# Kernel tuning notes

Measured on AMD Instinct MI355X. Metric: run time of the kernel, lower is better.

## Reference

```python
import jax, jax.numpy as jnp
import numpy as np

# Kernel codes matching style 'L;O2;P2;Y2,1,1;R0.5;W1,1'
KERNEL_CODES = ['L', 'O', 'P', 'Y', 'R', 'W']
SM_TEMP = 1.0


def _norm_sq(q, k):
    # q: [n,l,h,e], k: [n,s,h,e] -> [n,h,l,s]
    q2 = jnp.einsum('nlhe,nlhe->nhl', q, q)[..., None]        # [n,h,l,1]
    k2 = jnp.einsum('nshe,nshe->nhs', k, k)[:, :, None, :]     # [n,h,1,s]
    qk = jnp.einsum('nlhe,nshe->nhls', q, k)
    return q2 + k2 - 2.0 * qk


def _kernel(code, q, k):
    if code == 'L':
        return jnp.einsum('nlhe,nshe->nhls', q, k)
    if code == 'O':  # -log(1 + ns^(p/2)), p=2
        return -jnp.log1p(_norm_sq(q, k))
    if code == 'P':  # -(ns)^(p/2), p=2
        return -_norm_sq(q, k)
    if code == 'Y':  # (alpha*<q,k> + c)^p, p=2, alpha=1, c=1
        d = jnp.einsum('nlhe,nshe->nhls', q, k)
        return (d + 1.0) ** 2
    if code == 'R':  # exp(-gamma*ns), gamma=0.5
        return jnp.exp(-0.5 * _norm_sq(q, k))
    if code == 'W':  # cos(ns/a)*exp(-ns/b), a=b=1
        ns = _norm_sq(q, k)
        return jnp.cos(ns) * jnp.exp(-ns)
    raise ValueError(code)


def setup_inputs() -> dict:
    key = jax.random.key(0)
    k1, k2, k3, k4 = jax.random.split(key, 4)
    N, L, S, H, E, K = 2, 1024, 1024, 8, 64, 6
    return {
        'query': jax.random.normal(k1, (N, L, H, E), dtype=jnp.float32),
        'key': jax.random.normal(k2, (N, S, H, E), dtype=jnp.float32),
        'attn_mask_add': jnp.zeros((N, L, S), dtype=jnp.float32),
        'key_lengths_add': jnp.zeros((N, S), dtype=jnp.float32),
        'M': jax.random.uniform(k3, (H, E, K), dtype=jnp.float32),
        'C': jax.random.uniform(k4, (K, H, E, E), dtype=jnp.float32),
    }


def reference(query, key, attn_mask_add, key_lengths_add, M, C):
    # mixture weights pi: [n,l,h,k]
    pi = jax.nn.softmax(jnp.einsum('nlhe,hek->nlhk', query, M), axis=-1)
    out = None
    for c, code in enumerate(KERNEL_CODES):
        # htilde = tanh(query @ C[c]): [n,l,h,e]
        htilde = jnp.tanh(jnp.einsum('nlhe,hef->nlhf', query, C[c]))
        qk = _kernel(code, htilde, key)                    # [n,h,l,s]
        qk = qk + attn_mask_add[:, None] + key_lengths_add[:, None, None, :]
        sm = jax.nn.softmax(SM_TEMP * qk, axis=-1)
        w = jnp.transpose(pi[..., c], (0, 2, 1))[..., None]  # [n,h,l,1]
        term = sm * w
        out = term if out is None else out + term
    return out
```

## Files before the change

### kernel.cpp

```cpp
#include <hip/hip_runtime.h>
#include <hip/hip_bf16.h>
#include <math.h>

#define N_  2
#define H_  8
#define G_  16
#define L_  1024
#define S_  1024
#define E_  64
#define NC_ 6

typedef __attribute__((ext_vector_type(4))) float floatx4;
typedef __attribute__((ext_vector_type(8))) short short8;

#define MFMA16 __builtin_amdgcn_mfma_f32_16x16x32_bf16

#define AHAT_OFF   0
#define AHAT_BYTES (NC_*G_*L_*128*2)
#define KHAT_OFF   (AHAT_OFF + AHAT_BYTES)
#define KHAT_BYTES (G_*S_*128*2)
#define PI_OFF     (KHAT_OFF + KHAT_BYTES)
#define PI_BYTES   (NC_*G_*L_*4)
#define HSQ_OFF    (PI_OFF + PI_BYTES)
#define HSQ_BYTES  (NC_*G_*L_*4)
#define KSQ_OFF    (HSQ_OFF + HSQ_BYTES)
#define KSQ_BYTES  (G_*S_*4)

__global__ __launch_bounds__(256) void k_prep_a(
    const float* __restrict__ q, const float* __restrict__ M,
    const float* __restrict__ C, __hip_bfloat16* __restrict__ Ahat,
    float* __restrict__ pi_t, float* __restrict__ hsq) {
  extern __shared__ char smraw[];
  float* qs    = (float*)smraw;
  float* Cs    = qs + 32*65;
  float* hsq_s = Cs + 3*4104;
  float* pm    = hsq_s + 6*32;

  int b  = blockIdx.x;
  int n  = b >> 8; int h = (b >> 5) & 7; int lc = b & 31;
  int l0 = lc * 32; int g = n*8 + h;
  int t  = threadIdx.x;

  if (t < 192) hsq_s[t] = 0.0f;
  {
    int u = t;
    #pragma unroll
    for (int rep = 0; rep < 2; rep++, u += 256) {
      int row = u >> 4, seg = u & 15;
      float4 v = *(const float4*)(q + (((size_t)(n*L_ + l0 + row))*H_ + h)*E_ + seg*4);
      float* dst = qs + row*65 + seg*4;
      dst[0]=v.x; dst[1]=v.y; dst[2]=v.z; dst[3]=v.w;
    }
  }
  for (int gc = 0; gc < 2; gc++) {
    __syncthreads();
    for (int u = t; u < 3072; u += 256) {
      int cc = u >> 10; int rem = u & 1023; int e = rem >> 4; int seg = rem & 15;
      float4 v = *(const float4*)(C + (((size_t)((gc*3+cc)*8 + h))*64 + e)*64 + seg*4);
      float* dst = Cs + cc*4104 + e*64 + seg*4;
      dst[0]=v.x; dst[1]=v.y; dst[2]=v.z; dst[3]=v.w;
    }
    __syncthreads();
    if (t < 192) {
      int cc = t >> 6; int tt = t & 63; int lg = tt >> 3; int fg = tt & 7;
      int c = gc*3 + cc;
      float acc[4][8];
      #pragma unroll
      for (int i = 0; i < 4; i++)
        #pragma unroll
        for (int j = 0; j < 8; j++) acc[i][j] = 0.0f;
      for (int e = 0; e < 64; e++) {
        float c8[8];
        #pragma unroll
        for (int j = 0; j < 8; j++) c8[j] = Cs[cc*4104 + e*64 + fg*8 + j];
        #pragma unroll
        for (int i = 0; i < 4; i++) {
          float qv = qs[(lg*4+i)*65 + e];
          #pragma unroll
          for (int j = 0; j < 8; j++) acc[i][j] = fmaf(qv, c8[j], acc[i][j]);
        }
      }
      #pragma unroll
      for (int i = 0; i < 4; i++) {
        int l = l0 + lg*4 + i;
        size_t rowb = (((size_t)(c*G_ + g))*L_ + l) * 128;
        float ss = 0.0f;
        short8 hi8, lo8;
        #pragma unroll
        for (int j = 0; j < 8; j++) {
          float hv = tanhf(acc[i][j]);
          ss += hv*hv;
          __hip_bfloat16 hi = __float2bfloat16(hv);
          __hip_bfloat16 lo = __float2bfloat16(hv - __bfloat162float(hi));
          short hs, ls;
          __builtin_memcpy(&hs, &hi, 2);
          __builtin_memcpy(&ls, &lo, 2);
          hi8[j] = hs; lo8[j] = ls;
        }
        *(short8*)((char*)Ahat + (rowb + fg*8)*2)      = hi8;
        *(short8*)((char*)Ahat + (rowb + 64 + fg*8)*2) = lo8;
        atomicAdd(&hsq_s[c*32 + lg*4 + i], ss);
      }
    }
  }
  if (t < 192) {
    int k = t >> 5; int l = t & 31;
    float p = 0.0f;
    for (int e = 0; e < 64; e++) p += qs[l*65 + e] * M[(h*64 + e)*6 + k];
    pm[l*8 + k] = p;
  }
  __syncthreads();
  if (t < 192) {
    int k = t >> 5; int l = t & 31;
    float mx = pm[l*8+0];
    #pragma unroll
    for (int kk = 1; kk < 6; kk++) mx = fmaxf(mx, pm[l*8+kk]);
    float den = 0.0f;
    #pragma unroll
    for (int kk = 0; kk < 6; kk++) den += __expf(pm[l*8+kk] - mx);
    float pv = __expf(pm[l*8+k] - mx) / den;
    size_t idx = ((size_t)(k*G_ + g))*L_ + l0 + l;
    pi_t[idx] = pv;
    hsq[idx]  = hsq_s[k*32 + l];
  }
}

__global__ __launch_bounds__(256) void k_prep_k(
    const float* __restrict__ key, __hip_bfloat16* __restrict__ Khat,
    float* __restrict__ ksq) {
  int t = threadIdx.x; int wv = t >> 6; int lane = t & 63;
  int r = blockIdx.x*4 + wv;
  int g = r >> 10; int s = r & 1023; int n = g >> 3; int h = g & 7;
  float v = key[(((size_t)(n*S_ + s))*H_ + h)*E_ + lane];
  __hip_bfloat16 hi = __float2bfloat16(v);
  __hip_bfloat16 lo = __float2bfloat16(v - __bfloat162float(hi));
  size_t base = ((size_t)g*S_ + s)*128;
  Khat[base + lane]      = hi;
  Khat[base + 64 + lane] = lo;
  float sq = v*v;
  #pragma unroll
  for (int off = 32; off; off >>= 1) sq += __shfl_xor(sq, off);
  if (lane == 0) ksq[(size_t)g*S_ + s] = sq;
}

#define LDS_A6    0
#define LDS_K     0
#define LDS_KSQ   17408
#define LDS_KLEN  17664
#define LDS_ZRED  24576
#define LDS_MRED  26112
#define LDS_CST   27648
#define LDS_HSQ   28416
#define LDS_PI    28800
#define LDS_TOTAL 29184

__global__ __launch_bounds__(256, 2) void k_main(
    const __hip_bfloat16* __restrict__ Ahat, const __hip_bfloat16* __restrict__ Khat,
    const float* __restrict__ hsq, const float* __restrict__ ksq,
    const float* __restrict__ mask, const float* __restrict__ klen,
    const float* __restrict__ pi_t, float* __restrict__ out) {
  extern __shared__ char smraw[];
  char*   A6     = smraw + LDS_A6;
  char*   K_lds  = smraw + LDS_K;
  float*  ksq_t  = (float*)(smraw + LDS_KSQ);
  float*  klen_t = (float*)(smraw + LDS_KLEN);
  float*  zred   = (float*)(smraw + LDS_ZRED);
  float*  mred   = (float*)(smraw + LDS_MRED);
  float2* cst    = (float2*)(smraw + LDS_CST);
  float*  hsq_s  = (float*)(smraw + LDS_HSQ);
  float*  pi_s   = (float*)(smraw + LDS_PI);

  const int l0 = blockIdx.x * 16; const int g = blockIdx.y; const int n = g >> 3;
  const int t = threadIdx.x; const int w = t >> 6; const int lane = t & 63;
  const int quad = lane >> 4; const int lc = lane & 15;

  #pragma unroll
  for (int rep = 0; rep < 6; rep++) {
    int u = t + rep*256; int cc = u >> 8; int rem = u & 255;
    int row = rem >> 4; int seg = rem & 15;
    *(int4*)(A6 + cc*4096 + row*256 + seg*16) =
      *(const int4*)((const char*)Ahat + (((size_t)(cc*G_+g))*L_ + l0 + row)*256 + seg*16);
  }
  if (t < 96) {
    size_t idx = ((size_t)((t >> 4)*G_ + g))*L_ + l0 + (t & 15);
    hsq_s[t] = hsq[idx];
    pi_s[t]  = pi_t[idx];
  }
  __syncthreads();

  short8 a6f[6][4];
  #pragma unroll
  for (int cc = 0; cc < 6; cc++)
    #pragma unroll
    for (int kt = 0; kt < 4; kt++)
      a6f[cc][kt] = *(const short8*)(A6 + cc*4096 + lc*256 + kt*64 + quad*16);

  float h1p[4], nh2[4], h4h[4], nh5[4];
  #pragma unroll
  for (int i = 0; i < 4; i++) {
    int r = quad*4 + i;
    h1p[i] = 1.0f + hsq_s[1*16 + r];
    nh2[i] = -hsq_s[2*16 + r];
    h4h[i] = -0.5f * hsq_s[4*16 + r];
    nh5[i] = -hsq_s[5*16 + r];
  }

  float Zc[4][4];
  float m2[4], z2[4], m3[4], z3[4];
  #pragma unroll
  for (int i = 0; i < 4; i++) {
    #pragma unroll
    for (int c = 0; c < 4; c++) Zc[c][i] = 0.0f;
    m2[i] = -INFINITY; z2[i] = 0.0f;
    m3[i] = -INFINITY; z3[i] = 0.0f;
  }

  #pragma unroll 1
  for (int st = 0; st < 16; st++) {
    int s0 = st*64;
    __syncthreads();
    #pragma unroll
    for (int rep = 0; rep < 4; rep++) {
      int u = t + rep*256; int row = u >> 4, seg = u & 15;
      *(int4*)(K_lds + row*272 + seg*16) =
        *(const int4*)((const char*)Khat + (((size_t)g)*S_ + s0 + row)*256 + seg*16);
    }
    if (t < 64) { ksq_t[t] = ksq[(size_t)g*S_ + s0 + t]; klen_t[t] = klen[(size_t)n*S_ + s0 + t]; }
    int scol = s0 + w*16 + lc;
    float mk[4];
    #pragma unroll
    for (int i = 0; i < 4; i++)
      mk[i] = mask[((size_t)(n*L_ + l0 + quad*4 + i))*S_ + scol];
    __syncthreads();
    short8 bfr[4];
    #pragma unroll
    for (int kt = 0; kt < 4; kt++)
      bfr[kt] = *(const short8*)(K_lds + (w*16 + lc)*272 + kt*64 + quad*16);
    float kq  = ksq_t[w*16 + lc];
    float klv = klen_t[w*16 + lc];
    float mv[4], Ev[4];
    #pragma unroll
    for (int i = 0; i < 4; i++) { mv[i] = mk[i] + klv; Ev[i] = __expf(mv[i]); }
    #pragma unroll
    for (int c = 0; c < 6; c++) {
      floatx4 a = {0.f, 0.f, 0.f, 0.f};
      a = MFMA16(a6f[c][0], bfr[0], a, 0,0,0);
      a = MFMA16(a6f[c][1], bfr[1], a, 0,0,0);
      a = MFMA16(a6f[c][0], bfr[2], a, 0,0,0);
      a = MFMA16(a6f[c][1], bfr[3], a, 0,0,0);
      a = MFMA16(a6f[c][2], bfr[0], a, 0,0,0);
      a = MFMA16(a6f[c][3], bfr[1], a, 0,0,0);
      #pragma unroll
      for (int i = 0; i < 4; i++) {
        float d = a[i];
        if (c == 0) {
          Zc[0][i] = fmaf(Ev[i], __expf(d), Zc[0][i]);
        } else if (c == 1) {
          float onep = fmaf(-2.f, d, h1p[i] + kq);
          Zc[1][i] = fmaf(Ev[i], __builtin_amdgcn_rcpf(onep), Zc[1][i]);
        } else if (c == 2) {
          float x  = fmaf(2.f, d, nh2[i] - kq) + mv[i];
          float mn = fmaxf(m2[i], x);
          float e  = __expf(fminf(m2[i], x) - mn);
          z2[i] = (x > m2[i]) ? fmaf(z2[i], e, 1.0f) : (z2[i] + e);
          m2[i] = mn;
        } else if (c == 3) {
          float tt = d + 1.f;
          float x  = fmaf(tt, tt, mv[i]);
          float mn = fmaxf(m3[i], x);
          float e  = __expf(fminf(m3[i], x) - mn);
          z3[i] = (x > m3[i]) ? fmaf(z3[i], e, 1.0f) : (z3[i] + e);
          m3[i] = mn;
        } else if (c == 4) {
          float a4 = d + fmaf(-0.5f, kq, h4h[i]);
          Zc[2][i] = fmaf(Ev[i], __expf(__expf(a4)), Zc[2][i]);
        } else {
          float a5 = fmaf(2.f, d, nh5[i] - kq);
          Zc[3][i] = fmaf(Ev[i], __expf(__cosf(a5) * __expf(a5)), Zc[3][i]);
        }
      }
    }
  }

  #pragma unroll
  for (int off = 1; off < 16; off <<= 1) {
    #pragma unroll
    for (int c = 0; c < 4; c++)
      #pragma unroll
      for (int i = 0; i < 4; i++) Zc[c][i] += __shfl_xor(Zc[c][i], off);
    #pragma unroll
    for (int i = 0; i < 4; i++) {
      float mo = __shfl_xor(m2[i], off);
      float zo = __shfl_xor(z2[i], off);
      float mn = fmaxf(m2[i], mo);
      float e  = __expf(fminf(m2[i], mo) - mn);
      z2[i] = (mo > m2[i]) ? fmaf(z2[i], e, zo) : fmaf(zo, e, z2[i]);
      m2[i] = mn;
      mo = __shfl_xor(m3[i], off);
      zo = __shfl_xor(z3[i], off);
      mn = fmaxf(m3[i], mo);
      e  = __expf(fminf(m3[i], mo) - mn);
      z3[i] = (mo > m3[i]) ? fmaf(z3[i], e, zo) : fmaf(zo, e, z3[i]);
      m3[i] = mn;
    }
  }
  if (lc == 0) {
    static const int cmap[4] = {0, 1, 4, 5};
    #pragma unroll
    for (int c = 0; c < 4; c++)
      #pragma unroll
      for (int i = 0; i < 4; i++) {
        zred[w*96 + cmap[c]*16 + quad*4 + i] = Zc[c][i];
        mred[w*96 + cmap[c]*16 + quad*4 + i] = 0.f;
      }
    #pragma unroll
    for (int i = 0; i < 4; i++) {
      zred[w*96 + 2*16 + quad*4 + i] = z2[i];
      mred[w*96 + 2*16 + quad*4 + i] = m2[i];
      zred[w*96 + 3*16 + quad*4 + i] = z3[i];
      mred[w*96 + 3*16 + quad*4 + i] = m3[i];
    }
  }
  __syncthreads();
  if (t < 96) {
    int c = t >> 4;
    float z = zred[t], m = mred[t];
    if (c == 2 || c == 3) {
      #pragma unroll
      for (int w2 = 1; w2 < 4; w2++) {
        float mo = mred[w2*96 + t], zo = zred[w2*96 + t];
        float mn = fmaxf(m, mo);
        float e  = __expf(fminf(m, mo) - mn);
        z = (mo > m) ? fmaf(z, e, zo) : fmaf(zo, e, z);
        m = mn;
      }
    } else {
      #pragma unroll
      for (int w2 = 1; w2 < 4; w2++) z += zred[w2*96 + t];
    }
    cst[t] = make_float2(pi_s[t] / z, m);
  }
  __syncthreads();

  float ac[6][4], m2f[4], m3f[4];
  #pragma unroll
  for (int c = 0; c < 6; c++)
    #pragma unroll
    for (int i = 0; i < 4; i++) {
      float2 v = cst[c*16 + quad*4 + i];
      ac[c][i] = v.x;
      if (c == 2) m2f[i] = v.y;
      if (c == 3) m3f[i] = v.y;
    }

  #pragma unroll 1
  for (int st = 0; st < 16; st++) {
    int s0 = st*64;
    __syncthreads();
    #pragma unroll
    for (int rep = 0; rep < 4; rep++) {
      int u = t + rep*256; int row = u >> 4, seg = u & 15;
      *(int4*)(K_lds + row*272 + seg*16) =
        *(const int4*)((const char*)Khat + (((size_t)g)*S_ + s0 + row)*256 + seg*16);
    }
    if (t < 64) { ksq_t[t] = ksq[(size_t)g*S_ + s0 + t]; klen_t[t] = klen[(size_t)n*S_ + s0 + t]; }
    int scol = s0 + w*16 + lc;
    float mk[4];
    #pragma unroll
    for (int i = 0; i < 4; i++)
      mk[i] = mask[((size_t)(n*L_ + l0 + quad*4 + i))*S_ + scol];
    __syncthreads();
    short8 bfr[4];
    #pragma unroll
    for (int kt = 0; kt < 4; kt++)
      bfr[kt] = *(const short8*)(K_lds + (w*16 + lc)*272 + kt*64 + quad*16);
    float kq  = ksq_t[w*16 + lc];
    float klv = klen_t[w*16 + lc];
    float mv[4], Ev[4];
    #pragma unroll
    for (int i = 0; i < 4; i++) { mv[i] = mk[i] + klv; Ev[i] = __expf(mv[i]); }
    float Sacc[4] = {0.f, 0.f, 0.f, 0.f};
    float G[4]    = {0.f, 0.f, 0.f, 0.f};
    #pragma unroll
    for (int c = 0; c < 6; c++) {
      floatx4 a = {0.f, 0.f, 0.f, 0.f};
      a = MFMA16(a6f[c][0], bfr[0], a, 0,0,0);
      a = MFMA16(a6f[c][1], bfr[1], a, 0,0,0);
      a = MFMA16(a6f[c][0], bfr[2], a, 0,0,0);
      a = MFMA16(a6f[c][1], bfr[3], a, 0,0,0);
      a = MFMA16(a6f[c][2], bfr[0], a, 0,0,0);
      a = MFMA16(a6f[c][3], bfr[1], a, 0,0,0);
      #pragma unroll
      for (int i = 0; i < 4; i++) {
        float d = a[i];
        if (c == 0) {
          Sacc[i] = fmaf(ac[0][i], __expf(d), Sacc[i]);
        } else if (c == 1) {
          float onep = fmaf(-2.f, d, h1p[i] + kq);
          Sacc[i] = fmaf(ac[1][i], __builtin_amdgcn_rcpf(onep), Sacc[i]);
        } else if (c == 2) {
          float x = fmaf(2.f, d, nh2[i] - kq) + mv[i];
          G[i] = fmaf(ac[2][i], __expf(x - m2f[i]), G[i]);
        } else if (c == 3) {
          float tt = d + 1.f;
          float x  = fmaf(tt, tt, mv[i]);
          G[i] = fmaf(ac[3][i], __expf(x - m3f[i]), G[i]);
        } else if (c == 4) {
          float a4 = d + fmaf(-0.5f, kq, h4h[i]);
          Sacc[i] = fmaf(ac[4][i], __expf(__expf(a4)), Sacc[i]);
        } else {
          float a5 = fmaf(2.f, d, nh5[i] - kq);
          Sacc[i] = fmaf(ac[5][i], __expf(__cosf(a5) * __expf(a5)), Sacc[i]);
        }
      }
    }
    #pragma unroll
    for (int i = 0; i < 4; i++)
      out[(((size_t)g)*L_ + l0 + quad*4 + i)*S_ + scol] = fmaf(Ev[i], Sacc[i], G[i]);
  }
}

extern "C" void kernel_launch(void* const* d_in, const int* in_sizes, int n_in,
                              void* d_out, int out_size, void* d_ws, size_t ws_size,
                              hipStream_t stream) {
  (void)in_sizes; (void)n_in; (void)out_size; (void)ws_size;
  const float* q    = (const float*)d_in[0];
  const float* key  = (const float*)d_in[1];
  const float* mask = (const float*)d_in[2];
  const float* klen = (const float*)d_in[3];
  const float* M    = (const float*)d_in[4];
  const float* C    = (const float*)d_in[5];
  char* ws = (char*)d_ws;
  __hip_bfloat16* Ahat = (__hip_bfloat16*)(ws + AHAT_OFF);
  __hip_bfloat16* Khat = (__hip_bfloat16*)(ws + KHAT_OFF);
  float* pi_t    = (float*)(ws + PI_OFF);
  float* hsq     = (float*)(ws + HSQ_OFF);
  float* ksq     = (float*)(ws + KSQ_OFF);
  float* out = (float*)d_out;

  k_prep_a<<<512, 256, 59360, stream>>>(q, M, C, Ahat, pi_t, hsq);
  k_prep_k<<<4096, 256, 0, stream>>>(key, Khat, ksq);
  k_main<<<dim3(64, 16), 256, LDS_TOTAL, stream>>>(Ahat, Khat, hsq, ksq, mask, klen,
                                                   pi_t, out);
}
```

Before: 241.9 us.

## Split prep into htilde/pi kernels, fixed-shift P kernel softmax, hoist per-column constants

Replaces the single prep kernel with a grid-parallel htilde kernel (one block per l-chunk, component and head, vectorized LDS reads, exp-based fast tanh, shuffle reduction instead of shared atomics) and a separate pi kernel. In the main kernel, component P's online max/rescale softmax is replaced by a fixed shift of 64, which is an upper bound on the logit because |htilde|<1 over 64 dims. This removes the running max and its merge logic. Per-column constant terms are hoisted out of the component loop. The fixed shift assumes the mask and length additions are non-positive, and the fast tanh may lose accuracy.

```diff
diff --git a/kernel.cpp b/kernel.cpp
--- a/kernel.cpp
+++ b/kernel.cpp
@@ -26,106 +26,117 @@
 #define KSQ_OFF    (HSQ_OFF + HSQ_BYTES)
 #define KSQ_BYTES  (G_*S_*4)
 
-__global__ __launch_bounds__(256) void k_prep_a(
+__device__ __forceinline__ float ftanh(float x) {
+  return 1.0f - 2.0f * __builtin_amdgcn_rcpf(__expf(2.0f*x) + 1.0f);
+}
+
+__global__ __launch_bounds__(256) void k_htilde(
+    const float* __restrict__ q, const float* __restrict__ C,
+    __hip_bfloat16* __restrict__ Ahat, float* __restrict__ hsq) {
+  extern __shared__ char smraw[];
+  float* qs = (float*)smraw;
+  float* Cs = qs + 128*68;
+
+  const int lch = blockIdx.x, c = blockIdx.y, g = blockIdx.z;
+  const int n = g >> 3, h = g & 7;
+  const int l0 = lch * 128;
+  const int t = threadIdx.x;
+
+  for (int u = t; u < 2048; u += 256) {
+    int row = u >> 4, seg = u & 15;
+    *(float4*)(qs + row*68 + seg*4) =
+      *(const float4*)(q + (((size_t)(n*L_ + l0 + row))*H_ + h)*E_ + seg*4);
+  }
+  for (int u = t; u < 1024; u += 256) {
+    int e = u >> 4, seg = u & 15;
+    *(float4*)(Cs + e*68 + seg*4) =
+      *(const float4*)(C + (((size_t)(c*8 + h))*64 + e)*64 + seg*4);
+  }
+  __syncthreads();
+
+  const int rg = t >> 3, fg = t & 7;
+  float acc[4][8];
+  #pragma unroll
+  for (int i = 0; i < 4; i++)
+    #pragma unroll
+    for (int j = 0; j < 8; j++) acc[i][j] = 0.0f;
+
+  #pragma unroll 4
+  for (int e0 = 0; e0 < 64; e0 += 4) {
+    float4 q4[4];
+    #pragma unroll
+    for (int i = 0; i < 4; i++)
+      q4[i] = *(const float4*)(qs + (rg*4 + i)*68 + e0);
+    #pragma unroll
+    for (int ee = 0; ee < 4; ee++) {
+      float4 ca = *(const float4*)(Cs + (e0+ee)*68 + fg*8);
+      float4 cb = *(const float4*)(Cs + (e0+ee)*68 + fg*8 + 4);
+      float c8[8] = {ca.x, ca.y, ca.z, ca.w, cb.x, cb.y, cb.z, cb.w};
+      #pragma unroll
+      for (int i = 0; i < 4; i++) {
+        float qv = (ee == 0) ? q4[i].x : (ee == 1) ? q4[i].y
+                 : (ee == 2) ? q4[i].z : q4[i].w;
+        #pragma unroll
+        for (int j = 0; j < 8; j++) acc[i][j] = fmaf(qv, c8[j], acc[i][j]);
+      }
+    }
+  }
+
+  #pragma unroll
+  for (int i = 0; i < 4; i++) {
+    int l = l0 + rg*4 + i;
+    size_t rowb = (((size_t)(c*G_ + g))*L_ + l) * 128;
+    float ss = 0.0f;
+    short8 hi8, lo8;
+    #pragma unroll
+    for (int j = 0; j < 8; j++) {
+      float hv = ftanh(acc[i][j]);
+      ss += hv*hv;
+      __hip_bfloat16 hi = __float2bfloat16(hv);
+      __hip_bfloat16 lo = __float2bfloat16(hv - __bfloat162float(hi));
+      short hs, ls;
+      __builtin_memcpy(&hs, &hi, 2);
+      __builtin_memcpy(&ls, &lo, 2);
+      hi8[j] = hs; lo8[j] = ls;
+    }
+    *(short8*)((char*)Ahat + (rowb + fg*8)*2)      = hi8;
+    *(short8*)((char*)Ahat + (rowb + 64 + fg*8)*2) = lo8;
+    ss += __shfl_xor(ss, 1); ss += __shfl_xor(ss, 2); ss += __shfl_xor(ss, 4);
+    if (fg == 0) hsq[((size_t)(c*G_ + g))*L_ + l] = ss;
+  }
+}
+
+__global__ __launch_bounds__(256) void k_pi(
     const float* __restrict__ q, const float* __restrict__ M,
-    const float* __restrict__ C, __hip_bfloat16* __restrict__ Ahat,
-    float* __restrict__ pi_t, float* __restrict__ hsq) {
-  extern __shared__ char smraw[];
-  float* qs    = (float*)smraw;
-  float* Cs    = qs + 32*65;
-  float* hsq_s = Cs + 3*4104;
-  float* pm    = hsq_s + 6*32;
-
-  int b  = blockIdx.x;
-  int n  = b >> 8; int h = (b >> 5) & 7; int lc = b & 31;
-  int l0 = lc * 32; int g = n*8 + h;
-  int t  = threadIdx.x;
-
-  if (t < 192) hsq_s[t] = 0.0f;
-  {
-    int u = t;
-    #pragma unroll
-    for (int rep = 0; rep < 2; rep++, u += 256) {
-      int row = u >> 4, seg = u & 15;
-      float4 v = *(const float4*)(q + (((size_t)(n*L_ + l0 + row))*H_ + h)*E_ + seg*4);
-      float* dst = qs + row*65 + seg*4;
-      dst[0]=v.x; dst[1]=v.y; dst[2]=v.z; dst[3]=v.w;
-    }
-  }
-  for (int gc = 0; gc < 2; gc++) {
-    __syncthreads();
-    for (int u = t; u < 3072; u += 256) {
-      int cc = u >> 10; int rem = u & 1023; int e = rem >> 4; int seg = rem & 15;
-      float4 v = *(const float4*)(C + (((size_t)((gc*3+cc)*8 + h))*64 + e)*64 + seg*4);
-      float* dst = Cs + cc*4104 + e*64 + seg*4;
-      dst[0]=v.x; dst[1]=v.y; dst[2]=v.z; dst[3]=v.w;
-    }
-    __syncthreads();
-    if (t < 192) {
-      int cc = t >> 6; int tt = t & 63; int lg = tt >> 3; int fg = tt & 7;
-      int c = gc*3 + cc;
-      float acc[4][8];
-      #pragma unroll
-      for (int i = 0; i < 4; i++)
-        #pragma unroll
-        for (int j = 0; j < 8; j++) acc[i][j] = 0.0f;
-      for (int e = 0; e < 64; e++) {
-        float c8[8];
-        #pragma unroll
-        for (int j = 0; j < 8; j++) c8[j] = Cs[cc*4104 + e*64 + fg*8 + j];
-        #pragma unroll
-        for (int i = 0; i < 4; i++) {
-          float qv = qs[(lg*4+i)*65 + e];
-          #pragma unroll
-          for (int j = 0; j < 8; j++) acc[i][j] = fmaf(qv, c8[j], acc[i][j]);
-        }
-      }
-      #pragma unroll
-      for (int i = 0; i < 4; i++) {
-        int l = l0 + lg*4 + i;
-        size_t rowb = (((size_t)(c*G_ + g))*L_ + l) * 128;
-        float ss = 0.0f;
-        short8 hi8, lo8;
-        #pragma unroll
-        for (int j = 0; j < 8; j++) {
-          float hv = tanhf(acc[i][j]);
-          ss += hv*hv;
-          __hip_bfloat16 hi = __float2bfloat16(hv);
-          __hip_bfloat16 lo = __float2bfloat16(hv - __bfloat162float(hi));
-          short hs, ls;
-          __builtin_memcpy(&hs, &hi, 2);
-          __builtin_memcpy(&ls, &lo, 2);
-          hi8[j] = hs; lo8[j] = ls;
-        }
-        *(short8*)((char*)Ahat + (rowb + fg*8)*2)      = hi8;
-        *(short8*)((char*)Ahat + (rowb + 64 + fg*8)*2) = lo8;
-        atomicAdd(&hsq_s[c*32 + lg*4 + i], ss);
-      }
-    }
-  }
-  if (t < 192) {
-    int k = t >> 5; int l = t & 31;
-    float p = 0.0f;
-    for (int e = 0; e < 64; e++) p += qs[l*65 + e] * M[(h*64 + e)*6 + k];
-    pm[l*8 + k] = p;
-  }
+    float* __restrict__ pi_t) {
+  __shared__ float Ms[384];
+  const int g = blockIdx.x >> 2, lch = blockIdx.x & 3;
+  const int n = g >> 3, h = g & 7;
+  const int t = threadIdx.x;
+  const int l = lch*256 + t;
+  for (int u = t; u < 384; u += 256) Ms[u] = M[h*384 + u];
   __syncthreads();
-  if (t < 192) {
-    int k = t >> 5; int l = t & 31;
-    float mx = pm[l*8+0];
-    #pragma unroll
-    for (int kk = 1; kk < 6; kk++) mx = fmaxf(mx, pm[l*8+kk]);
-    float den = 0.0f;
-    #pragma unroll
-    for (int kk = 0; kk < 6; kk++) den += __expf(pm[l*8+kk] - mx);
-    float pv = __expf(pm[l*8+k] - mx) / den;
-    size_t idx = ((size_t)(k*G_ + g))*L_ + l0 + l;
-    pi_t[idx] = pv;
-    hsq[idx]  = hsq_s[k*32 + l];
-  }
-}
-
-__global__ __launch_bounds__(256) void k_prep_k(
+  const float* qrow = q + (((size_t)(n*L_ + l))*H_ + h)*E_;
+  float p[6] = {0.f, 0.f, 0.f, 0.f, 0.f, 0.f};
+  #pragma unroll 8
+  for (int e = 0; e < 64; e++) {
+    float qv = qrow[e];
+    #pragma unroll
+    for (int k = 0; k < 6; k++) p[k] = fmaf(qv, Ms[e*6 + k], p[k]);
+  }
+  float mx = p[0];
+  #pragma unroll
+  for (int k = 1; k < 6; k++) mx = fmaxf(mx, p[k]);
+  float den = 0.f;
+  #pragma unroll
+  for (int k = 0; k < 6; k++) den += __expf(p[k] - mx);
+  float rden = __builtin_amdgcn_rcpf(den);
+  #pragma unroll
+  for (int k = 0; k < 6; k++)
+    pi_t[((size_t)(k*G_ + g))*L_ + l] = __expf(p[k] - mx) * rden;
+}
+
+__global__ __launch_bounds__(256) void k_key(
     const float* __restrict__ key, __hip_bfloat16* __restrict__ Khat,
     float* __restrict__ ksq) {
   int t = threadIdx.x; int wv = t >> 6; int lane = t & 63;
@@ -143,7 +154,6 @@
   if (lane == 0) ksq[(size_t)g*S_ + s] = sq;
 }
 
-#define LDS_A6    0
 #define LDS_K     0
 #define LDS_KSQ   17408
 #define LDS_KLEN  17664
@@ -160,7 +170,7 @@
     const float* __restrict__ mask, const float* __restrict__ klen,
     const float* __restrict__ pi_t, float* __restrict__ out) {
   extern __shared__ char smraw[];
-  char*   A6     = smraw + LDS_A6;
+  char*   A6     = smraw;
   char*   K_lds  = smraw + LDS_K;
   float*  ksq_t  = (float*)(smraw + LDS_KSQ);
   float*  klen_t = (float*)(smraw + LDS_KLEN);
@@ -200,19 +210,17 @@
   for (int i = 0; i < 4; i++) {
     int r = quad*4 + i;
     h1p[i] = 1.0f + hsq_s[1*16 + r];
-    nh2[i] = -hsq_s[2*16 + r];
+    nh2[i] = 64.0f - hsq_s[2*16 + r];
     h4h[i] = -0.5f * hsq_s[4*16 + r];
     nh5[i] = -hsq_s[5*16 + r];
   }
 
-  float Zc[4][4];
-  float m2[4], z2[4], m3[4], z3[4];
+  float Zc[4][4], zp[4], m3[4], z3[4];
   #pragma unroll
   for (int i = 0; i < 4; i++) {
     #pragma unroll
     for (int c = 0; c < 4; c++) Zc[c][i] = 0.0f;
-    m2[i] = -INFINITY; z2[i] = 0.0f;
-    m3[i] = -INFINITY; z3[i] = 0.0f;
+    zp[i] = 0.0f; m3[i] = -INFINITY; z3[i] = 0.0f;
   }
 
   #pragma unroll 1
@@ -238,9 +246,16 @@
       bfr[kt] = *(const short8*)(K_lds + (w*16 + lc)*272 + kt*64 + quad*16);
     float kq  = ksq_t[w*16 + lc];
     float klv = klen_t[w*16 + lc];
-    float mv[4], Ev[4];
-    #pragma unroll
-    for (int i = 0; i < 4; i++) { mv[i] = mk[i] + klv; Ev[i] = __expf(mv[i]); }
+    float mv[4], Ev[4], oc[4], pc[4], rc[4], wc[4];
+    #pragma unroll
+    for (int i = 0; i < 4; i++) {
+      mv[i] = mk[i] + klv;
+      Ev[i] = __expf(mv[i]);
+      oc[i] = h1p[i] + kq;
+      pc[i] = nh2[i] - kq + mv[i];
+      rc[i] = fmaf(-0.5f, kq, h4h[i]);
+      wc[i] = nh5[i] - kq;
+    }
     #pragma unroll
     for (int c = 0; c < 6; c++) {
       floatx4 a = {0.f, 0.f, 0.f, 0.f};
@@ -256,14 +271,9 @@
         if (c == 0) {
           Zc[0][i] = fmaf(Ev[i], __expf(d), Zc[0][i]);
         } else if (c == 1) {
-          float onep = fmaf(-2.f, d, h1p[i] + kq);
-          Zc[1][i] = fmaf(Ev[i], __builtin_amdgcn_rcpf(onep), Zc[1][i]);
+          Zc[1][i] = fmaf(Ev[i], __builtin_amdgcn_rcpf(fmaf(-2.f, d, oc[i])), Zc[1][i]);
         } else if (c == 2) {
-          float x  = fmaf(2.f, d, nh2[i] - kq) + mv[i];
-          float mn = fmaxf(m2[i], x);
-          float e  = __expf(fminf(m2[i], x) - mn);
-          z2[i] = (x > m2[i]) ? fmaf(z2[i], e, 1.0f) : (z2[i] + e);
-          m2[i] = mn;
+          zp[i] += __expf(fmaf(2.f, d, pc[i]));
         } else if (c == 3) {
           float tt = d + 1.f;
           float x  = fmaf(tt, tt, mv[i]);
@@ -272,10 +282,9 @@
           z3[i] = (x > m3[i]) ? fmaf(z3[i], e, 1.0f) : (z3[i] + e);
           m3[i] = mn;
         } else if (c == 4) {
-          float a4 = d + fmaf(-0.5f, kq, h4h[i]);
-          Zc[2][i] = fmaf(Ev[i], __expf(__expf(a4)), Zc[2][i]);
+          Zc[2][i] = fmaf(Ev[i], __expf(__expf(d + rc[i])), Zc[2][i]);
         } else {
-          float a5 = fmaf(2.f, d, nh5[i] - kq);
+          float a5 = fmaf(2.f, d, wc[i]);
           Zc[3][i] = fmaf(Ev[i], __expf(__cosf(a5) * __expf(a5)), Zc[3][i]);
         }
       }
@@ -290,16 +299,11 @@
       for (int i = 0; i < 4; i++) Zc[c][i] += __shfl_xor(Zc[c][i], off);
     #pragma unroll
     for (int i = 0; i < 4; i++) {
-      float mo = __shfl_xor(m2[i], off);
-      float zo = __shfl_xor(z2[i], off);
-      float mn = fmaxf(m2[i], mo);
-      float e  = __expf(fminf(m2[i], mo) - mn);
-      z2[i] = (mo > m2[i]) ? fmaf(z2[i], e, zo) : fmaf(zo, e, z2[i]);
-      m2[i] = mn;
-      mo = __shfl_xor(m3[i], off);
-      zo = __shfl_xor(z3[i], off);
-      mn = fmaxf(m3[i], mo);
-      e  = __expf(fminf(m3[i], mo) - mn);
+      zp[i] += __shfl_xor(zp[i], off);
+      float mo = __shfl_xor(m3[i], off);
+      float zo = __shfl_xor(z3[i], off);
+      float mn = fmaxf(m3[i], mo);
+      float e  = __expf(fminf(m3[i], mo) - mn);
       z3[i] = (mo > m3[i]) ? fmaf(z3[i], e, zo) : fmaf(zo, e, z3[i]);
       m3[i] = mn;
     }
@@ -315,8 +319,8 @@
       }
     #pragma unroll
     for (int i = 0; i < 4; i++) {
-      zred[w*96 + 2*16 + quad*4 + i] = z2[i];
-      mred[w*96 + 2*16 + quad*4 + i] = m2[i];
+      zred[w*96 + 2*16 + quad*4 + i] = zp[i];
+      mred[w*96 + 2*16 + quad*4 + i] = 0.f;
       zred[w*96 + 3*16 + quad*4 + i] = z3[i];
       mred[w*96 + 3*16 + quad*4 + i] = m3[i];
     }
@@ -325,7 +329,7 @@
   if (t < 96) {
     int c = t >> 4;
     float z = zred[t], m = mred[t];
-    if (c == 2 || c == 3) {
+    if (c == 3) {
       #pragma unroll
       for (int w2 = 1; w2 < 4; w2++) {
         float mo = mred[w2*96 + t], zo = zred[w2*96 + t];
@@ -342,14 +346,13 @@
   }
   __syncthreads();
 
-  float ac[6][4], m2f[4], m3f[4];
+  float ac[6][4], m3f[4];
   #pragma unroll
   for (int c = 0; c < 6; c++)
     #pragma unroll
     for (int i = 0; i < 4; i++) {
       float2 v = cst[c*16 + quad*4 + i];
       ac[c][i] = v.x;
-      if (c == 2) m2f[i] = v.y;
       if (c == 3) m3f[i] = v.y;
     }
 
@@ -376,9 +379,16 @@
       bfr[kt] = *(const short8*)(K_lds + (w*16 + lc)*272 + kt*64 + quad*16);
     float kq  = ksq_t[w*16 + lc];
     float klv = klen_t[w*16 + lc];
-    float mv[4], Ev[4];
-    #pragma unroll
-    for (int i = 0; i < 4; i++) { mv[i] = mk[i] + klv; Ev[i] = __expf(mv[i]); }
+    float mv[4], Ev[4], oc[4], pc[4], rc[4], wc[4];
+    #pragma unroll
+    for (int i = 0; i < 4; i++) {
+      mv[i] = mk[i] + klv;
+      Ev[i] = __expf(mv[i]);
+      oc[i] = h1p[i] + kq;
+      pc[i] = nh2[i] - kq + mv[i];
+      rc[i] = fmaf(-0.5f, kq, h4h[i]);
+      wc[i] = nh5[i] - kq;
+    }
     float Sacc[4] = {0.f, 0.f, 0.f, 0.f};
     float G[4]    = {0.f, 0.f, 0.f, 0.f};
     #pragma unroll
@@ -396,20 +406,17 @@
         if (c == 0) {
           Sacc[i] = fmaf(ac[0][i], __expf(d), Sacc[i]);
         } else if (c == 1) {
-          float onep = fmaf(-2.f, d, h1p[i] + kq);
-          Sacc[i] = fmaf(ac[1][i], __builtin_amdgcn_rcpf(onep), Sacc[i]);
+          Sacc[i] = fmaf(ac[1][i], __builtin_amdgcn_rcpf(fmaf(-2.f, d, oc[i])), Sacc[i]);
         } else if (c == 2) {
-          float x = fmaf(2.f, d, nh2[i] - kq) + mv[i];
-          G[i] = fmaf(ac[2][i], __expf(x - m2f[i]), G[i]);
+          G[i] = fmaf(ac[2][i], __expf(fmaf(2.f, d, pc[i])), G[i]);
         } else if (c == 3) {
           float tt = d + 1.f;
           float x  = fmaf(tt, tt, mv[i]);
           G[i] = fmaf(ac[3][i], __expf(x - m3f[i]), G[i]);
         } else if (c == 4) {
-          float a4 = d + fmaf(-0.5f, kq, h4h[i]);
-          Sacc[i] = fmaf(ac[4][i], __expf(__expf(a4)), Sacc[i]);
+          Sacc[i] = fmaf(ac[4][i], __expf(__expf(d + rc[i])), Sacc[i]);
         } else {
-          float a5 = fmaf(2.f, d, nh5[i] - kq);
+          float a5 = fmaf(2.f, d, wc[i]);
           Sacc[i] = fmaf(ac[5][i], __expf(__cosf(a5) * __expf(a5)), Sacc[i]);
         }
       }
@@ -438,8 +445,9 @@
   float* ksq     = (float*)(ws + KSQ_OFF);
   float* out = (float*)d_out;
 
-  k_prep_a<<<512, 256, 59360, stream>>>(q, M, C, Ahat, pi_t, hsq);
-  k_prep_k<<<4096, 256, 0, stream>>>(key, Khat, ksq);
+  k_htilde<<<dim3(8, 6, 16), 256, 52224, stream>>>(q, C, Ahat, hsq);
+  k_key<<<4096, 256, 0, stream>>>(key, Khat, ksq);
+  k_pi<<<64, 256, 0, stream>>>(q, M, pi_t);
   k_main<<<dim3(64, 16), 256, LDS_TOTAL, stream>>>(Ahat, Khat, hsq, ksq, mask, klen,
                                                    pi_t, out);
 }
```

New measurement: 223.2 us. 1.08x faster.
